# Kernel tuning notes

Hardware: AMD Instinct MI355X
Metric: run time of the kernel (lower is better)

Reference implementation:

```python
import jax, jax.numpy as jnp
import numpy as np

TEMPERATURE = 0.1  # use_temperature=True


def setup_inputs() -> dict:
    key = jax.random.key(0)
    # encoder output features: [batch_size, num_epoch, feature_dim]
    feature = jax.random.normal(key, (128, 64, 128), dtype=jnp.float32)
    return {"feature": feature}


def reference(feature):
    # L2-normalize along feature dim (F.normalize, p=2, dim=1 on flat features)
    f = feature / jnp.linalg.norm(feature, axis=-1, keepdims=True)
    B, E, D = f.shape
    # full pairwise logits: [B, E, E, B]
    logits = jnp.einsum('ijk,mnk->ijnm', f, f) / TEMPERATURE
    e = jnp.exp(logits)
    idx = jnp.arange(B)
    # mask[i, j, :, i] = 1 -> positives are the m == i block: e[i, j, :, i]
    pos = e[idx, :, :, idx].sum(-1)              # [B, E]
    neg = e.sum(axis=(2, 3)) - pos               # [B, E] everything else
    loss = (-jnp.log(pos / (pos + neg))).mean()
    return loss
```

## Files before the change

kernel.cpp:

```cpp
#include <hip/hip_runtime.h>
#include <hip/hip_bf16.h>

#define N_ROWS 8192
#define DIM    128
#define TILE   128
#define PADH   136
#define CPG    8
#define EXPTEN 22026.465794806718f

typedef __attribute__((ext_vector_type(8))) short short8;
typedef __attribute__((ext_vector_type(4))) float floatx4;

__global__ void norm_kernel(const float* __restrict__ F, __hip_bfloat16* __restrict__ Xb) {
    int lane = threadIdx.x & 63;
    int wave = threadIdx.x >> 6;
    int row  = blockIdx.x * 4 + wave;
    const float2 v = *(const float2*)(F + (size_t)row * DIM + lane * 2);
    float ss = v.x * v.x + v.y * v.y;
    #pragma unroll
    for (int m = 1; m < 64; m <<= 1) ss += __shfl_xor(ss, m);
    float inv = rsqrtf(ss);
    __hip_bfloat162 o;
    o.x = __float2bfloat16(v.x * inv);
    o.y = __float2bfloat16(v.y * inv);
    *((__hip_bfloat162*)(Xb + (size_t)row * DIM) + lane) = o;
}

__global__ __launch_bounds__(256, 2) void gram_kernel(
        const __hip_bfloat16* __restrict__ Xb,
        float* __restrict__ pos, float* __restrict__ den) {
    __shared__ __hip_bfloat16 As[TILE * PADH];
    __shared__ __hip_bfloat16 Bs[TILE * PADH];
    const int tid  = threadIdx.x;
    const int rb   = blockIdx.x;
    const int cg   = blockIdx.y;
    const int lane = tid & 63;
    const int wave = tid >> 6;
    const int wm   = wave >> 1, wn = wave & 1;
    const int quad = lane >> 4;
    const int l15  = lane & 15;

    #pragma unroll
    for (int it = 0; it < 8; ++it) {
        int idx = it * 256 + tid;
        int row = idx >> 4, c8 = idx & 15;
        float4 t = *(const float4*)(Xb + ((size_t)(rb * TILE + row)) * DIM + c8 * 8);
        *(float4*)((char*)As + row * (PADH * 2) + c8 * 16) = t;
    }

    float dp[4][4], pp[4][4];
    #pragma unroll
    for (int a = 0; a < 4; ++a)
        #pragma unroll
        for (int b = 0; b < 4; ++b) { dp[a][b] = 0.f; pp[a][b] = 0.f; }

    for (int t = 0; t < CPG; ++t) {
        const int ct = cg * CPG + t;
        __syncthreads();
        #pragma unroll
        for (int it = 0; it < 8; ++it) {
            int idx = it * 256 + tid;
            int row = idx >> 4, c8 = idx & 15;
            float4 v = *(const float4*)(Xb + ((size_t)(ct * TILE + row)) * DIM + c8 * 8);
            *(float4*)((char*)Bs + row * (PADH * 2) + c8 * 16) = v;
        }
        __syncthreads();

        floatx4 acc[4][4];
        #pragma unroll
        for (int mi = 0; mi < 4; ++mi)
            #pragma unroll
            for (int ni = 0; ni < 4; ++ni) acc[mi][ni] = (floatx4)0.0f;

        #pragma unroll
        for (int ko = 0; ko < 4; ++ko) {
            short8 af[4], bf[4];
            #pragma unroll
            for (int mi = 0; mi < 4; ++mi) {
                int r = wm * 64 + mi * 16 + l15;
                af[mi] = *(const short8*)((const char*)As + r * (PADH * 2) + ko * 64 + quad * 16);
            }
            #pragma unroll
            for (int ni = 0; ni < 4; ++ni) {
                int r = wn * 64 + ni * 16 + l15;
                bf[ni] = *(const short8*)((const char*)Bs + r * (PADH * 2) + ko * 64 + quad * 16);
            }
            #pragma unroll
            for (int mi = 0; mi < 4; ++mi)
                #pragma unroll
                for (int ni = 0; ni < 4; ++ni)
                    acc[mi][ni] = __builtin_amdgcn_mfma_f32_16x16x32_bf16(
                        af[mi], bf[ni], acc[mi][ni], 0, 0, 0);
        }

        const bool pos_tile = (ct == rb) && (wm == wn);
        #pragma unroll
        for (int mi = 0; mi < 4; ++mi)
            #pragma unroll
            for (int rg = 0; rg < 4; ++rg) {
                float dadd = 0.f;
                #pragma unroll
                for (int ni = 0; ni < 4; ++ni)
                    dadd += __expf(acc[mi][ni][rg] * 10.0f);
                if (pos_tile) {
                    if (l15 == quad * 4 + rg)
                        dadd += EXPTEN - __expf(acc[mi][mi][rg] * 10.0f);
                    pp[mi][rg] += dadd;
                }
                dp[mi][rg] += dadd;
            }
    }

    const bool has_pos = (wm == wn) && ((rb >> 3) == cg);
    #pragma unroll
    for (int mi = 0; mi < 4; ++mi)
        #pragma unroll
        for (int rg = 0; rg < 4; ++rg) {
            float d = dp[mi][rg];
            #pragma unroll
            for (int m = 1; m < 16; m <<= 1) d += __shfl_xor(d, m);
            int grow = rb * TILE + wm * 64 + mi * 16 + quad * 4 + rg;
            if (l15 == 0) atomicAdd(&den[grow], d);
            if (has_pos) {
                float p = pp[mi][rg];
                #pragma unroll
                for (int m = 1; m < 16; m <<= 1) p += __shfl_xor(p, m);
                if (l15 == 0) atomicAdd(&pos[grow], p);
            }
        }
}

__global__ void loss_kernel(const float* __restrict__ pos, const float* __restrict__ den,
                            float* __restrict__ out) {
    __shared__ float red[4];
    float acc = 0.f;
    for (int r = threadIdx.x; r < N_ROWS; r += 256)
        acc += __logf(den[r] / pos[r]);
    #pragma unroll
    for (int m = 1; m < 64; m <<= 1) acc += __shfl_xor(acc, m);
    int lane = threadIdx.x & 63, w = threadIdx.x >> 6;
    if (lane == 0) red[w] = acc;
    __syncthreads();
    if (threadIdx.x == 0)
        out[0] = (red[0] + red[1] + red[2] + red[3]) * (1.0f / (float)N_ROWS);
}

extern "C" void kernel_launch(void* const* d_in, const int* in_sizes, int n_in,
                              void* d_out, int out_size, void* d_ws, size_t ws_size,
                              hipStream_t stream) {
    const float* feature = (const float*)d_in[0];
    float* pos = (float*)d_ws;
    float* den = pos + N_ROWS;
    __hip_bfloat16* Xb = (__hip_bfloat16*)(den + N_ROWS);

    hipMemsetAsync(d_ws, 0, 2 * N_ROWS * sizeof(float), stream);
    norm_kernel<<<N_ROWS / 4, 256, 0, stream>>>(feature, Xb);
    gram_kernel<<<dim3(64, 8), 256, 0, stream>>>(Xb, pos, den);
    loss_kernel<<<1, 256, 0, stream>>>(pos, den, (float*)d_out);
}
```

Before: 96.45 us.

## Load MFMA fragments directly from global, pipeline epilogue, fold scale into normalization

Replaces LDS staging and barriers in the Gram kernel with direct global-to-register fragment loads. The next tile's load overlaps the current tile's exp epilogue. Inputs are pre-scaled by sqrt(10*log2 e), so the epilogue uses a raw exp2 with no multiply. The workspace memset is folded into the normalization kernel and the loss kernel uses vector loads. This trades LDS reuse for more L2 traffic and higher register pressure.

```diff
diff --git a/kernel.cpp b/kernel.cpp
--- a/kernel.cpp
+++ b/kernel.cpp
@@ -4,14 +4,21 @@
 #define N_ROWS 8192
 #define DIM    128
 #define TILE   128
-#define PADH   136
 #define CPG    8
 #define EXPTEN 22026.465794806718f
+#define SCALE  3.7982826f
 
 typedef __attribute__((ext_vector_type(8))) short short8;
 typedef __attribute__((ext_vector_type(4))) float floatx4;
 
-__global__ void norm_kernel(const float* __restrict__ F, __hip_bfloat16* __restrict__ Xb) {
+#if __has_builtin(__builtin_amdgcn_exp2f)
+#define EXP2F(x) __builtin_amdgcn_exp2f(x)
+#else
+#define EXP2F(x) __expf((x) * 0.6931471805599453f)
+#endif
+
+__global__ void norm_kernel(const float* __restrict__ F, __hip_bfloat16* __restrict__ Xb,
+                            float* __restrict__ pos, float* __restrict__ den) {
     int lane = threadIdx.x & 63;
     int wave = threadIdx.x >> 6;
     int row  = blockIdx.x * 4 + wave;
@@ -19,18 +26,17 @@
     float ss = v.x * v.x + v.y * v.y;
     #pragma unroll
     for (int m = 1; m < 64; m <<= 1) ss += __shfl_xor(ss, m);
-    float inv = rsqrtf(ss);
+    float inv = rsqrtf(ss) * SCALE;
     __hip_bfloat162 o;
     o.x = __float2bfloat16(v.x * inv);
     o.y = __float2bfloat16(v.y * inv);
     *((__hip_bfloat162*)(Xb + (size_t)row * DIM) + lane) = o;
+    if (lane == 0) { pos[row] = 0.f; den[row] = 0.f; }
 }
 
 __global__ __launch_bounds__(256, 2) void gram_kernel(
         const __hip_bfloat16* __restrict__ Xb,
         float* __restrict__ pos, float* __restrict__ den) {
-    __shared__ __hip_bfloat16 As[TILE * PADH];
-    __shared__ __hip_bfloat16 Bs[TILE * PADH];
     const int tid  = threadIdx.x;
     const int rb   = blockIdx.x;
     const int cg   = blockIdx.y;
@@ -40,59 +46,26 @@
     const int quad = lane >> 4;
     const int l15  = lane & 15;
 
-    #pragma unroll
-    for (int it = 0; it < 8; ++it) {
-        int idx = it * 256 + tid;
-        int row = idx >> 4, c8 = idx & 15;
-        float4 t = *(const float4*)(Xb + ((size_t)(rb * TILE + row)) * DIM + c8 * 8);
-        *(float4*)((char*)As + row * (PADH * 2) + c8 * 16) = t;
+    short8 af[4][4];
+    {
+        const __hip_bfloat16* Ab = Xb + ((size_t)(rb * TILE + wm * 64 + l15)) * DIM + quad * 8;
+        #pragma unroll
+        for (int mi = 0; mi < 4; ++mi)
+            #pragma unroll
+            for (int ko = 0; ko < 4; ++ko)
+                af[mi][ko] = *(const short8*)(Ab + mi * 16 * DIM + ko * 32);
     }
 
-    float dp[4][4], pp[4][4];
+    float dp[4][4];
     #pragma unroll
     for (int a = 0; a < 4; ++a)
         #pragma unroll
-        for (int b = 0; b < 4; ++b) { dp[a][b] = 0.f; pp[a][b] = 0.f; }
+        for (int b = 0; b < 4; ++b) dp[a][b] = 0.f;
 
-    for (int t = 0; t < CPG; ++t) {
-        const int ct = cg * CPG + t;
-        __syncthreads();
-        #pragma unroll
-        for (int it = 0; it < 8; ++it) {
-            int idx = it * 256 + tid;
-            int row = idx >> 4, c8 = idx & 15;
-            float4 v = *(const float4*)(Xb + ((size_t)(ct * TILE + row)) * DIM + c8 * 8);
-            *(float4*)((char*)Bs + row * (PADH * 2) + c8 * 16) = v;
-        }
-        __syncthreads();
+    floatx4 acc[4][4];
+    short8 bfr[4][4];
 
-        floatx4 acc[4][4];
-        #pragma unroll
-        for (int mi = 0; mi < 4; ++mi)
-            #pragma unroll
-            for (int ni = 0; ni < 4; ++ni) acc[mi][ni] = (floatx4)0.0f;
-
-        #pragma unroll
-        for (int ko = 0; ko < 4; ++ko) {
-            short8 af[4], bf[4];
-            #pragma unroll
-            for (int mi = 0; mi < 4; ++mi) {
-                int r = wm * 64 + mi * 16 + l15;
-                af[mi] = *(const short8*)((const char*)As + r * (PADH * 2) + ko * 64 + quad * 16);
-            }
-            #pragma unroll
-            for (int ni = 0; ni < 4; ++ni) {
-                int r = wn * 64 + ni * 16 + l15;
-                bf[ni] = *(const short8*)((const char*)Bs + r * (PADH * 2) + ko * 64 + quad * 16);
-            }
-            #pragma unroll
-            for (int mi = 0; mi < 4; ++mi)
-                #pragma unroll
-                for (int ni = 0; ni < 4; ++ni)
-                    acc[mi][ni] = __builtin_amdgcn_mfma_f32_16x16x32_bf16(
-                        af[mi], bf[ni], acc[mi][ni], 0, 0, 0);
-        }
-
+    auto epilogue = [&](int ct) {
         const bool pos_tile = (ct == rb) && (wm == wn);
         #pragma unroll
         for (int mi = 0; mi < 4; ++mi)
@@ -101,17 +74,54 @@
                 float dadd = 0.f;
                 #pragma unroll
                 for (int ni = 0; ni < 4; ++ni)
-                    dadd += __expf(acc[mi][ni][rg] * 10.0f);
+                    dadd += EXP2F(acc[mi][ni][rg]);
                 if (pos_tile) {
                     if (l15 == quad * 4 + rg)
-                        dadd += EXPTEN - __expf(acc[mi][mi][rg] * 10.0f);
-                    pp[mi][rg] += dadd;
+                        dadd += EXPTEN - EXP2F(acc[mi][mi][rg]);
+                    float p = dadd;
+                    #pragma unroll
+                    for (int m = 1; m < 16; m <<= 1) p += __shfl_xor(p, m);
+                    if (l15 == 0)
+                        atomicAdd(&pos[rb * TILE + wm * 64 + mi * 16 + quad * 4 + rg], p);
                 }
                 dp[mi][rg] += dadd;
             }
+    };
+
+    auto load_b = [&](int ct) {
+        const __hip_bfloat16* Bb = Xb + ((size_t)(ct * TILE + wn * 64 + l15)) * DIM + quad * 8;
+        #pragma unroll
+        for (int ni = 0; ni < 4; ++ni)
+            #pragma unroll
+            for (int ko = 0; ko < 4; ++ko)
+                bfr[ni][ko] = *(const short8*)(Bb + ni * 16 * DIM + ko * 32);
+    };
+
+    auto do_mfma = [&]() {
+        #pragma unroll
+        for (int mi = 0; mi < 4; ++mi)
+            #pragma unroll
+            for (int ni = 0; ni < 4; ++ni) acc[mi][ni] = (floatx4)0.0f;
+        #pragma unroll
+        for (int ko = 0; ko < 4; ++ko)
+            #pragma unroll
+            for (int mi = 0; mi < 4; ++mi)
+                #pragma unroll
+                for (int ni = 0; ni < 4; ++ni)
+                    acc[mi][ni] = __builtin_amdgcn_mfma_f32_16x16x32_bf16(
+                        af[mi][ko], bfr[ni][ko], acc[mi][ni], 0, 0, 0);
+    };
+
+    load_b(cg * CPG);
+    do_mfma();
+    #pragma unroll 1
+    for (int t = 1; t < CPG; ++t) {
+        load_b(cg * CPG + t);
+        epilogue(cg * CPG + t - 1);
+        do_mfma();
     }
+    epilogue(cg * CPG + CPG - 1);
 
-    const bool has_pos = (wm == wn) && ((rb >> 3) == cg);
     #pragma unroll
     for (int mi = 0; mi < 4; ++mi)
         #pragma unroll
@@ -119,14 +129,8 @@
             float d = dp[mi][rg];
             #pragma unroll
             for (int m = 1; m < 16; m <<= 1) d += __shfl_xor(d, m);
-            int grow = rb * TILE + wm * 64 + mi * 16 + quad * 4 + rg;
-            if (l15 == 0) atomicAdd(&den[grow], d);
-            if (has_pos) {
-                float p = pp[mi][rg];
-                #pragma unroll
-                for (int m = 1; m < 16; m <<= 1) p += __shfl_xor(p, m);
-                if (l15 == 0) atomicAdd(&pos[grow], p);
-            }
+            if (l15 == 0)
+                atomicAdd(&den[rb * TILE + wm * 64 + mi * 16 + quad * 4 + rg], d);
         }
 }
 
@@ -134,8 +138,12 @@
                             float* __restrict__ out) {
     __shared__ float red[4];
     float acc = 0.f;
-    for (int r = threadIdx.x; r < N_ROWS; r += 256)
-        acc += __logf(den[r] / pos[r]);
+    for (int i = threadIdx.x; i < N_ROWS / 4; i += 256) {
+        float4 d = ((const float4*)den)[i];
+        float4 p = ((const float4*)pos)[i];
+        acc += __logf(d.x / p.x) + __logf(d.y / p.y) +
+               __logf(d.z / p.z) + __logf(d.w / p.w);
+    }
     #pragma unroll
     for (int m = 1; m < 64; m <<= 1) acc += __shfl_xor(acc, m);
     int lane = threadIdx.x & 63, w = threadIdx.x >> 6;
@@ -153,8 +161,7 @@
     float* den = pos + N_ROWS;
     __hip_bfloat16* Xb = (__hip_bfloat16*)(den + N_ROWS);
 
-    hipMemsetAsync(d_ws, 0, 2 * N_ROWS * sizeof(float), stream);
-    norm_kernel<<<N_ROWS / 4, 256, 0, stream>>>(feature, Xb);
+    norm_kernel<<<N_ROWS / 4, 256, 0, stream>>>(feature, Xb, pos, den);
     gram_kernel<<<dim3(64, 8), 256, 0, stream>>>(Xb, pos, den);
     loss_kernel<<<1, 256, 0, stream>>>(pos, den, (float*)d_out);
 }
```

Result: slower. 99.97 us (+3.6%).
